# Performance work log

Hardware: AMD Instinct MI355X
Metric: run time of the kernel (lower is better)

## Reference

```python
import jax, jax.numpy as jnp
import numpy as np

E = 8_000_000  # n_edges
B = 4096       # n_graphs

def setup_inputs() -> dict:
    key = jax.random.key(0)
    ks = jax.random.split(key, 9)
    src = jax.random.normal(ks[0], (E, 1), dtype=jnp.float32)
    dest = jax.random.normal(ks[1], (E, 1), dtype=jnp.float32)
    edge_attr = jax.random.normal(ks[2], (E, 1), dtype=jnp.float32)
    u = jax.random.normal(ks[3], (B, 1), dtype=jnp.float32)
    batch = jax.random.randint(ks[4], (E,), 0, B, dtype=jnp.int64)
    # edge_mlp params: Lin(4,10) -> ReLU -> Lin(10,19)
    W1 = jax.random.normal(ks[5], (4, 10), dtype=jnp.float32) * (1.0 / np.sqrt(4))
    b1 = jnp.zeros((10,), dtype=jnp.float32)
    W2 = jax.random.normal(ks[6], (10, 19), dtype=jnp.float32) * (1.0 / np.sqrt(10))
    b2 = jnp.zeros((19,), dtype=jnp.float32)
    return {"src": src, "dest": dest, "edge_attr": edge_attr, "u": u,
            "batch": batch, "W1": W1, "b1": b1, "W2": W2, "b2": b2}

def reference(src, dest, edge_attr, u, batch, W1, b1, W2, b2):
    # gather per-graph global state to edges, concat along feature dim
    x = jnp.concatenate([src, dest, edge_attr, u[batch]], axis=1)  # [E, 4]
    h = jax.nn.relu(x @ W1 + b1)                                   # [E, 10]
    return h @ W2 + b2                                             # [E, 19]
```

## Files before the change

### kernel.cpp

```cpp
#include <hip/hip_runtime.h>

#define THREADS 256
#define EPT     2
#define F_HID   10
#define F_OUT   19
#define WAVEW   64
#define EPW     (WAVEW * EPT)
#define SLAB    (EPW * F_OUT)
#define NW      (THREADS / WAVEW)

typedef float f32x2 __attribute__((ext_vector_type(2)));
typedef float f32x4 __attribute__((ext_vector_type(4)));
typedef int   i32x2 __attribute__((ext_vector_type(2)));

__device__ __forceinline__ void mlp1(float x0, float x1, float x2, float x3,
                                     const float* __restrict__ W1,
                                     const float* __restrict__ b1,
                                     const float* __restrict__ W2,
                                     const float* __restrict__ b2,
                                     float* __restrict__ o)
{
    #pragma unroll
    for (int k = 0; k < F_OUT; ++k) o[k] = b2[k];
    #pragma unroll
    for (int j = 0; j < F_HID; ++j) {
        float a = b1[j];
        a = fmaf(x0, W1[0 * F_HID + j], a);
        a = fmaf(x1, W1[1 * F_HID + j], a);
        a = fmaf(x2, W1[2 * F_HID + j], a);
        a = fmaf(x3, W1[3 * F_HID + j], a);
        a = fmaxf(a, 0.0f);
        #pragma unroll
        for (int k = 0; k < F_OUT; ++k)
            o[k] = fmaf(a, W2[j * F_OUT + k], o[k]);
    }
}

__global__ __launch_bounds__(THREADS) void edge_mlp_kernel(
    const float* __restrict__ src,
    const float* __restrict__ dst,
    const float* __restrict__ ea,
    const float* __restrict__ u,
    const int*   __restrict__ batch,
    const float* __restrict__ W1,
    const float* __restrict__ b1,
    const float* __restrict__ W2,
    const float* __restrict__ b2,
    float* __restrict__ out,
    int n_edges)
{
    __shared__ float lds[NW * SLAB];

    const int tid  = threadIdx.x;
    const int lane = tid & (WAVEW - 1);
    const int wv   = tid >> 6;
    const int bs   = blockIdx.x * (THREADS * EPT);

    if (bs + THREADS * EPT <= n_edges) {
        const int e0 = bs + wv * EPW + lane * EPT;

        const f32x2 xs = *(const f32x2*)(src + e0);
        const f32x2 xd = *(const f32x2*)(dst + e0);
        const f32x2 xa = *(const f32x2*)(ea  + e0);
        const i32x2 bi = *(const i32x2*)(batch + e0);
        f32x2 xu; xu.x = u[bi.x]; xu.y = u[bi.y];

        float o[EPT * F_OUT];
        #pragma unroll
        for (int k = 0; k < F_OUT; ++k) { o[k] = b2[k]; o[F_OUT + k] = b2[k]; }

        #pragma unroll
        for (int j = 0; j < F_HID; ++j) {
            const float w0 = W1[0 * F_HID + j];
            const float w1 = W1[1 * F_HID + j];
            const float w2 = W1[2 * F_HID + j];
            const float w3 = W1[3 * F_HID + j];
            const float bb = b1[j];

            float a0 = fmaf(xu.x, w3, bb);
            a0 = fmaf(xa.x, w2, a0);
            a0 = fmaf(xd.x, w1, a0);
            a0 = fmaf(xs.x, w0, a0);
            a0 = fmaxf(a0, 0.0f);

            float a1 = fmaf(xu.y, w3, bb);
            a1 = fmaf(xa.y, w2, a1);
            a1 = fmaf(xd.y, w1, a1);
            a1 = fmaf(xs.y, w0, a1);
            a1 = fmaxf(a1, 0.0f);

            #pragma unroll
            for (int k = 0; k < F_OUT; ++k) {
                const float w = W2[j * F_OUT + k];
                o[k]         = fmaf(a0, w, o[k]);
                o[F_OUT + k] = fmaf(a1, w, o[F_OUT + k]);
            }
        }

        float* slab = lds + wv * SLAB;
        {
            f32x2* my = (f32x2*)(slab + lane * (EPT * F_OUT));
            #pragma unroll
            for (int p = 0; p < (EPT * F_OUT) / 2; ++p) {
                f32x2 t;
                t.x = o[2 * p];
                t.y = o[2 * p + 1];
                my[p] = t;
            }
        }
        __builtin_amdgcn_wave_barrier();

        {
            const f32x4* sv = (const f32x4*)slab;
            f32x4* ov = (f32x4*)(out + (size_t)(bs + wv * EPW) * F_OUT);
            for (int idx = lane; idx < SLAB / 4; idx += WAVEW)
                __builtin_nontemporal_store(sv[idx], ov + idx);
        }
    } else {
        const int e0 = bs + wv * EPW + lane * EPT;
        #pragma unroll
        for (int r = 0; r < EPT; ++r) {
            const int e = e0 + r;
            if (e < n_edges) {
                float o[F_OUT];
                mlp1(src[e], dst[e], ea[e], u[batch[e]], W1, b1, W2, b2, o);
                #pragma unroll
                for (int k = 0; k < F_OUT; ++k)
                    out[(size_t)e * F_OUT + k] = o[k];
            }
        }
    }
}

extern "C" void kernel_launch(void* const* d_in, const int* in_sizes, int n_in,
                              void* d_out, int out_size, void* d_ws, size_t ws_size,
                              hipStream_t stream) {
    const float* src   = (const float*)d_in[0];
    const float* dst   = (const float*)d_in[1];
    const float* ea    = (const float*)d_in[2];
    const float* u     = (const float*)d_in[3];
    const int*   batch = (const int*)  d_in[4];
    const float* W1    = (const float*)d_in[5];
    const float* b1    = (const float*)d_in[6];
    const float* W2    = (const float*)d_in[7];
    const float* b2    = (const float*)d_in[8];
    float* out = (float*)d_out;

    const int n = in_sizes[0];
    const int edges_per_block = THREADS * EPT;
    const int blocks = (n + edges_per_block - 1) / edges_per_block;
    edge_mlp_kernel<<<blocks, THREADS, 0, stream>>>(
        src, dst, ea, u, batch, W1, b1, W2, b2, out, n);
}
```

Baseline: 701.8 us.

## Use persistent grid-stride blocks with software-prefetched next-chunk inputs

Replaces the one-block-per-chunk launch with a grid capped at 1024 blocks. Each block loops over chunks with a grid stride and loads the next chunk's src, dst, edge_attr and batch values while it computes and stores the current chunk. The aim is to hide input load latency and cut block launch overhead in this memory-bound kernel. In exchange it uses more registers for the prefetch buffers, adds an occupancy hint of 4 in launch_bounds, and only 1024 blocks may not give enough waves in flight to saturate HBM bandwidth.

```diff
diff --git a/kernel.cpp b/kernel.cpp
--- a/kernel.cpp
+++ b/kernel.cpp
@@ -6,8 +6,10 @@
 #define F_OUT   19
 #define WAVEW   64
 #define EPW     (WAVEW * EPT)
+#define CHUNK   (THREADS * EPT)
 #define SLAB    (EPW * F_OUT)
 #define NW      (THREADS / WAVEW)
+#define MAXBLK  1024
 
 typedef float f32x2 __attribute__((ext_vector_type(2)));
 typedef float f32x4 __attribute__((ext_vector_type(4)));
@@ -36,7 +38,7 @@
     }
 }
 
-__global__ __launch_bounds__(THREADS) void edge_mlp_kernel(
+__global__ __launch_bounds__(THREADS, 4) void edge_mlp_kernel(
     const float* __restrict__ src,
     const float* __restrict__ dst,
     const float* __restrict__ ea,
@@ -54,81 +56,112 @@
     const int tid  = threadIdx.x;
     const int lane = tid & (WAVEW - 1);
     const int wv   = tid >> 6;
-    const int bs   = blockIdx.x * (THREADS * EPT);
+    const int NC   = (n_edges + CHUNK - 1) / CHUNK;
 
-    if (bs + THREADS * EPT <= n_edges) {
-        const int e0 = bs + wv * EPW + lane * EPT;
+    int c = blockIdx.x;
+    if (c >= NC) return;
 
-        const f32x2 xs = *(const f32x2*)(src + e0);
-        const f32x2 xd = *(const f32x2*)(dst + e0);
-        const f32x2 xa = *(const f32x2*)(ea  + e0);
-        const i32x2 bi = *(const i32x2*)(batch + e0);
-        f32x2 xu; xu.x = u[bi.x]; xu.y = u[bi.y];
+    const int loff = wv * EPW + lane * EPT;
+    float* slab = lds + wv * SLAB;
 
-        float o[EPT * F_OUT];
-        #pragma unroll
-        for (int k = 0; k < F_OUT; ++k) { o[k] = b2[k]; o[F_OUT + k] = b2[k]; }
+    f32x2 xs, xd, xa; i32x2 bi;
+    bool cur_full = ((long)c * CHUNK + CHUNK <= (long)n_edges);
+    if (cur_full) {
+        const int e0 = c * CHUNK + loff;
+        xs = *(const f32x2*)(src + e0);
+        xd = *(const f32x2*)(dst + e0);
+        xa = *(const f32x2*)(ea  + e0);
+        bi = *(const i32x2*)(batch + e0);
+    }
 
-        #pragma unroll
-        for (int j = 0; j < F_HID; ++j) {
-            const float w0 = W1[0 * F_HID + j];
-            const float w1 = W1[1 * F_HID + j];
-            const float w2 = W1[2 * F_HID + j];
-            const float w3 = W1[3 * F_HID + j];
-            const float bb = b1[j];
+    while (true) {
+        const int  cn        = c + gridDim.x;
+        const bool has_next  = (cn < NC);
+        const bool next_full = has_next &&
+                               ((long)cn * CHUNK + CHUNK <= (long)n_edges);
 
-            float a0 = fmaf(xu.x, w3, bb);
-            a0 = fmaf(xa.x, w2, a0);
-            a0 = fmaf(xd.x, w1, a0);
-            a0 = fmaf(xs.x, w0, a0);
-            a0 = fmaxf(a0, 0.0f);
+        f32x2 nxs, nxd, nxa; i32x2 nbi;
+        if (next_full) {
+            const int e1 = cn * CHUNK + loff;
+            nxs = *(const f32x2*)(src + e1);
+            nxd = *(const f32x2*)(dst + e1);
+            nxa = *(const f32x2*)(ea  + e1);
+            nbi = *(const i32x2*)(batch + e1);
+        }
 
-            float a1 = fmaf(xu.y, w3, bb);
-            a1 = fmaf(xa.y, w2, a1);
-            a1 = fmaf(xd.y, w1, a1);
-            a1 = fmaf(xs.y, w0, a1);
-            a1 = fmaxf(a1, 0.0f);
+        if (cur_full) {
+            f32x2 xu; xu.x = u[bi.x]; xu.y = u[bi.y];
+
+            float o[EPT * F_OUT];
+            #pragma unroll
+            for (int k = 0; k < F_OUT; ++k) { o[k] = b2[k]; o[F_OUT + k] = b2[k]; }
 
             #pragma unroll
-            for (int k = 0; k < F_OUT; ++k) {
-                const float w = W2[j * F_OUT + k];
-                o[k]         = fmaf(a0, w, o[k]);
-                o[F_OUT + k] = fmaf(a1, w, o[F_OUT + k]);
+            for (int j = 0; j < F_HID; ++j) {
+                const float w0 = W1[0 * F_HID + j];
+                const float w1 = W1[1 * F_HID + j];
+                const float w2 = W1[2 * F_HID + j];
+                const float w3 = W1[3 * F_HID + j];
+                const float bb = b1[j];
+
+                float a0 = bb;
+                a0 = fmaf(xs.x, w0, a0);
+                a0 = fmaf(xd.x, w1, a0);
+                a0 = fmaf(xa.x, w2, a0);
+                a0 = fmaf(xu.x, w3, a0);
+                a0 = fmaxf(a0, 0.0f);
+
+                float a1 = bb;
+                a1 = fmaf(xs.y, w0, a1);
+                a1 = fmaf(xd.y, w1, a1);
+                a1 = fmaf(xa.y, w2, a1);
+                a1 = fmaf(xu.y, w3, a1);
+                a1 = fmaxf(a1, 0.0f);
+
+                #pragma unroll
+                for (int k = 0; k < F_OUT; ++k) {
+                    const float w = W2[j * F_OUT + k];
+                    o[k]         = fmaf(a0, w, o[k]);
+                    o[F_OUT + k] = fmaf(a1, w, o[F_OUT + k]);
+                }
+            }
+
+            {
+                f32x2* my = (f32x2*)(slab + lane * (EPT * F_OUT));
+                #pragma unroll
+                for (int p = 0; p < (EPT * F_OUT) / 2; ++p) {
+                    f32x2 t;
+                    t.x = o[2 * p];
+                    t.y = o[2 * p + 1];
+                    my[p] = t;
+                }
+            }
+            __builtin_amdgcn_wave_barrier();
+
+            {
+                const f32x4* sv = (const f32x4*)slab;
+                f32x4* ov = (f32x4*)(out + (size_t)(c * CHUNK + wv * EPW) * F_OUT);
+                for (int idx = lane; idx < SLAB / 4; idx += WAVEW)
+                    __builtin_nontemporal_store(sv[idx], ov + idx);
+            }
+        } else {
+            #pragma unroll
+            for (int r = 0; r < EPT; ++r) {
+                const int e = c * CHUNK + loff + r;
+                if (e < n_edges) {
+                    float o[F_OUT];
+                    mlp1(src[e], dst[e], ea[e], u[batch[e]], W1, b1, W2, b2, o);
+                    #pragma unroll
+                    for (int k = 0; k < F_OUT; ++k)
+                        out[(size_t)e * F_OUT + k] = o[k];
+                }
             }
         }
 
-        float* slab = lds + wv * SLAB;
-        {
-            f32x2* my = (f32x2*)(slab + lane * (EPT * F_OUT));
-            #pragma unroll
-            for (int p = 0; p < (EPT * F_OUT) / 2; ++p) {
-                f32x2 t;
-                t.x = o[2 * p];
-                t.y = o[2 * p + 1];
-                my[p] = t;
-            }
-        }
-        __builtin_amdgcn_wave_barrier();
-
-        {
-            const f32x4* sv = (const f32x4*)slab;
-            f32x4* ov = (f32x4*)(out + (size_t)(bs + wv * EPW) * F_OUT);
-            for (int idx = lane; idx < SLAB / 4; idx += WAVEW)
-                __builtin_nontemporal_store(sv[idx], ov + idx);
-        }
-    } else {
-        const int e0 = bs + wv * EPW + lane * EPT;
-        #pragma unroll
-        for (int r = 0; r < EPT; ++r) {
-            const int e = e0 + r;
-            if (e < n_edges) {
-                float o[F_OUT];
-                mlp1(src[e], dst[e], ea[e], u[batch[e]], W1, b1, W2, b2, o);
-                #pragma unroll
-                for (int k = 0; k < F_OUT; ++k)
-                    out[(size_t)e * F_OUT + k] = o[k];
-            }
-        }
+        if (!has_next) break;
+        c = cn;
+        cur_full = next_full;
+        if (next_full) { xs = nxs; xd = nxd; xa = nxa; bi = nbi; }
     }
 }
 
@@ -146,9 +179,9 @@
     const float* b2    = (const float*)d_in[8];
     float* out = (float*)d_out;
 
-    const int n = in_sizes[0];
-    const int edges_per_block = THREADS * EPT;
-    const int blocks = (n + edges_per_block - 1) / edges_per_block;
+    const int n  = in_sizes[0];
+    const int NC = (n + CHUNK - 1) / CHUNK;
+    const int blocks = NC < MAXBLK ? NC : MAXBLK;
     edge_mlp_kernel<<<blocks, THREADS, 0, stream>>>(
         src, dst, ea, u, batch, W1, b1, W2, b2, out, n);
 }
```

After: 730.9 us. +4.1%, slower.
